# Performance work log

Hardware: AMD Instinct MI355X
Metric: run time of the kernel (lower is better)

## Reference

```python
import jax, jax.numpy as jnp
import numpy as np

B, N, H, D = 2, 2048, 8, 64  # batch, seq, heads, out_channels (per-head, incl. time dim)
E = H * 64                   # embed dim = num_heads * in_channels
C = 1.0                      # manifold curvature c
EPS = 1e-8


def setup_inputs() -> dict:
    key = jax.random.key(0)
    ks = jax.random.split(key, 8)
    d_out = H * (D - 1)
    inp = {
        "query_input": jax.random.normal(ks[0], (B, N, E), dtype=jnp.float32),
        "source_input": jax.random.normal(ks[1], (B, N, E), dtype=jnp.float32),
        "Wq_w": jax.random.normal(ks[2], (d_out, E), dtype=jnp.float32) * 0.02,
        "Wq_b": jnp.zeros((d_out,), dtype=jnp.float32),
        "Wk_w": jax.random.normal(ks[3], (d_out, E), dtype=jnp.float32) * 0.02,
        "Wk_b": jnp.zeros((d_out,), dtype=jnp.float32),
        "Wv_w": jax.random.normal(ks[4], (d_out, E), dtype=jnp.float32) * 0.02,
        "Wv_b": jnp.zeros((d_out,), dtype=jnp.float32),
        "scale": jnp.array([np.sqrt(H * D)], dtype=jnp.float32),
        "bias": jnp.zeros((), dtype=jnp.float32),
    }
    return inp


def _lift(x_space):
    # project space coords onto hyperboloid: prepend time = sqrt(||x||^2 + c)
    t = jnp.sqrt(jnp.sum(x_space * x_space, axis=-1, keepdims=True) + C)
    return jnp.concatenate([t, x_space], axis=-1)  # [..., D]


def _centroid(ave):
    # Lorentzian centroid normalization: sqrt(c) * ave / sqrt(|<ave,ave>_L|)
    inner = jnp.sum(ave * ave, axis=-1, keepdims=True) - 2.0 * ave[..., :1] ** 2
    denom = jnp.sqrt(jnp.maximum(jnp.abs(inner), EPS))
    return jnp.sqrt(C) * ave / denom


def reference(query_input, source_input, Wq_w, Wq_b, Wk_w, Wk_b, Wv_w, Wv_b, scale, bias):
    def heads(x, W, b):
        return (x @ W.T + b).reshape(B, N, H, D - 1)

    q = _lift(heads(query_input, Wq_w, Wq_b))   # [B,N,H,D]
    k = _lift(heads(source_input, Wk_w, Wk_b))  # [B,N,H,D]
    v = _lift(heads(source_input, Wv_w, Wv_b))  # [B,N,H,D]

    # Lorentzian inner product: negate time component of q
    sign = jnp.concatenate([-jnp.ones((1,), q.dtype), jnp.ones((D - 1,), q.dtype)])
    att = 2.0 * C + 2.0 * jnp.einsum('bnhd,bmhd->bhnm', q * sign, k)  # [B,H,N,N]
    att = att / scale[0] + bias
    w = jax.nn.softmax(att, axis=-1)

    ave = jnp.einsum('bhnm,bmhd->bnhd', w, v)   # weighted sum of values
    out = _centroid(ave)                         # per-head hyperbolic centroid [B,N,H,D]
    out = _centroid(jnp.mean(out, axis=2))       # centroid across heads -> [B,N,D]
    return out
```

## Files before the change

kernel.cpp:

```cpp
#include <hip/hip_runtime.h>
#include <math.h>
#include <stdint.h>

#define BB   2
#define NN   2048
#define HH   8
#define DD   64
#define EE   512
#define DM1  63
#define KSP  4

typedef _Float16 half8  __attribute__((ext_vector_type(8)));
typedef __fp16   fp16x2 __attribute__((ext_vector_type(2)));
typedef float    floatx4 __attribute__((ext_vector_type(4)));

__device__ __forceinline__ uint32_t pkh2(float a, float b) {
    union { fp16x2 h; uint32_t u; } uu;
    uu.h = __builtin_amdgcn_cvt_pkrtz(a, b);
    return uu.u;
}
__device__ __forceinline__ half8 as_half8(uint4 u) {
    union { uint4 u; half8 h; } uu; uu.u = u; return uu.h;
}

__global__ __launch_bounds__(256, 3) void qkv_mfma(
    const float* __restrict__ Xq, const float* __restrict__ Xs,
    const float* __restrict__ Wq, const float* __restrict__ Wk,
    const float* __restrict__ Wv,
    const float* __restrict__ Wqb, const float* __restrict__ Wkb,
    const float* __restrict__ Wvb, const float* __restrict__ scale_p,
    _Float16* __restrict__ q16, _Float16* __restrict__ k16,
    _Float16* __restrict__ vT16)
{
    const int mtb = blockIdx.x;
    const int hp  = blockIdx.y;
    const int mat = blockIdx.z;
    const int t    = threadIdx.x;
    const int w    = t >> 6;
    const int lane = t & 63;
    const int l15  = lane & 15;
    const int quad = lane >> 4;

    __shared__ alignas(16) char smem[27648];
    __shared__ float psum[64][4];
    _Float16 (*Xsh)[72]  = (_Float16(*)[72])smem;
    _Float16 (*Wsh)[72]  = (_Float16(*)[72])(smem + 9216);
    _Float16 (*Osh)[136] = (_Float16(*)[136])(smem + 9216);
    _Float16 (*OshT)[72] = (_Float16(*)[72])(smem + 9216);

    const float* X    = (mat == 0) ? Xq : Xs;
    const float* W    = (mat == 0) ? Wq : (mat == 1 ? Wk : Wv);
    const float* bias = (mat == 0) ? Wqb : (mat == 1 ? Wkb : Wvb);
    const int tok0 = mtb * 64;

    floatx4 acc[4][2];
#pragma unroll
    for (int mt = 0; mt < 4; mt++)
#pragma unroll
        for (int nt = 0; nt < 2; nt++) acc[mt][nt] = (floatx4){0.f,0.f,0.f,0.f};

    float4 pxa[2], pxb[2], pwa[4], pwb[4];
#pragma unroll
    for (int ls = 0; ls < 2; ls++) {
        int g = t + 256 * ls, r = g >> 3, c = g & 7;
        const float* p = X + (size_t)(tok0 + r) * EE + c * 8;
        pxa[ls] = *(const float4*)p;
        pxb[ls] = *(const float4*)(p + 4);
    }
#pragma unroll
    for (int ls = 0; ls < 4; ls++) {
        int g = t + 256 * ls, r = g >> 3, c = g & 7;
        int head = r >> 6, j = r & 63;
        pwa[ls] = make_float4(0.f,0.f,0.f,0.f);
        pwb[ls] = make_float4(0.f,0.f,0.f,0.f);
        if (j < DM1) {
            const float* p = W + (size_t)((hp * 2 + head) * DM1 + j) * EE + c * 8;
            pwa[ls] = *(const float4*)p;
            pwb[ls] = *(const float4*)(p + 4);
        }
    }

    for (int it = 0; it < 8; it++) {
        __syncthreads();
#pragma unroll
        for (int ls = 0; ls < 2; ls++) {
            int g = t + 256 * ls, r = g >> 3, c = g & 7;
            uint4 h;
            h.x = pkh2(pxa[ls].x, pxa[ls].y); h.y = pkh2(pxa[ls].z, pxa[ls].w);
            h.z = pkh2(pxb[ls].x, pxb[ls].y); h.w = pkh2(pxb[ls].z, pxb[ls].w);
            *(uint4*)&Xsh[r][c * 8] = h;
        }
#pragma unroll
        for (int ls = 0; ls < 4; ls++) {
            int g = t + 256 * ls, r = g >> 3, c = g & 7;
            uint4 h;
            h.x = pkh2(pwa[ls].x, pwa[ls].y); h.y = pkh2(pwa[ls].z, pwa[ls].w);
            h.z = pkh2(pwb[ls].x, pwb[ls].y); h.w = pkh2(pwb[ls].z, pwb[ls].w);
            *(uint4*)&Wsh[r][c * 8] = h;
        }
        __syncthreads();
        if (it + 1 < 8) {
            int ek = (it + 1) * 64;
#pragma unroll
            for (int ls = 0; ls < 2; ls++) {
                int g = t + 256 * ls, r = g >> 3, c = g & 7;
                const float* p = X + (size_t)(tok0 + r) * EE + ek + c * 8;
                pxa[ls] = *(const float4*)p;
                pxb[ls] = *(const float4*)(p + 4);
            }
#pragma unroll
            for (int ls = 0; ls < 4; ls++) {
                int g = t + 256 * ls, r = g >> 3, c = g & 7;
                int head = r >> 6, j = r & 63;
                if (j < DM1) {
                    const float* p = W + (size_t)((hp * 2 + head) * DM1 + j) * EE + ek + c * 8;
                    pwa[ls] = *(const float4*)p;
                    pwb[ls] = *(const float4*)(p + 4);
                }
            }
        }
#pragma unroll
        for (int kk = 0; kk < 2; kk++) {
            half8 a[4];
#pragma unroll
            for (int mt = 0; mt < 4; mt++)
                a[mt] = *(const half8*)&Xsh[mt * 16 + l15][kk * 32 + quad * 8];
#pragma unroll
            for (int nt = 0; nt < 2; nt++) {
                half8 bfr = *(const half8*)&Wsh[w * 32 + nt * 16 + l15][kk * 32 + quad * 8];
#pragma unroll
                for (int mt = 0; mt < 4; mt++)
                    acc[mt][nt] = __builtin_amdgcn_mfma_f32_16x16x32_f16(
                        a[mt], bfr, acc[mt][nt], 0, 0, 0);
            }
        }
    }
    __syncthreads();

    const float st   = 2.0f / scale_p[0];
    const float fmul = (mat == 0) ? st : 1.0f;

    float vals[4][2][4];
    float sqp[4][4];
#pragma unroll
    for (int mt = 0; mt < 4; mt++)
#pragma unroll
        for (int r = 0; r < 4; r++) sqp[mt][r] = 0.f;

#pragma unroll
    for (int mt = 0; mt < 4; mt++)
#pragma unroll
        for (int nt = 0; nt < 2; nt++) {
            int col = w * 32 + nt * 16 + l15;
            int head = col >> 6, j = col & 63;
            float bb = (j < DM1) ? bias[(hp * 2 + head) * DM1 + j] : 0.f;
#pragma unroll
            for (int r = 0; r < 4; r++) {
                float vv = acc[mt][nt][r] + bb;
                if (j >= DM1) vv = 0.f;
                vals[mt][nt][r] = vv;
                sqp[mt][r] += vv * vv;
            }
        }
#pragma unroll
    for (int mt = 0; mt < 4; mt++)
#pragma unroll
        for (int r = 0; r < 4; r++) {
            float s = sqp[mt][r];
            s += __shfl_xor(s, 1, 64); s += __shfl_xor(s, 2, 64);
            s += __shfl_xor(s, 4, 64); s += __shfl_xor(s, 8, 64);
            if (l15 == 0) psum[mt * 16 + quad * 4 + r][w] = s;
        }

    if (mat < 2) {
#pragma unroll
        for (int mt = 0; mt < 4; mt++)
#pragma unroll
            for (int nt = 0; nt < 2; nt++) {
                int col = w * 32 + nt * 16 + l15;
                int head = col >> 6, j = col & 63;
                if (j < DM1) {
                    int dc = head * 64 + 1 + j;
#pragma unroll
                    for (int r = 0; r < 4; r++)
                        Osh[mt * 16 + quad * 4 + r][dc] = (_Float16)(vals[mt][nt][r] * fmul);
                }
            }
    } else {
#pragma unroll
        for (int mt = 0; mt < 4; mt++)
#pragma unroll
            for (int nt = 0; nt < 2; nt++) {
                int col = w * 32 + nt * 16 + l15;
                uint2 pu;
                pu.x = pkh2(vals[mt][nt][0], vals[mt][nt][1]);
                pu.y = pkh2(vals[mt][nt][2], vals[mt][nt][3]);
                *(uint2*)&OshT[col][mt * 16 + quad * 4] = pu;
            }
    }
    __syncthreads();
    if (t < 64) {
        float tsA = sqrtf(psum[t][0] + psum[t][1] + 1.0f);
        float tsB = sqrtf(psum[t][2] + psum[t][3] + 1.0f);
        if (mat < 2) {
            float tm = (mat == 0) ? -st : 1.0f;
            Osh[t][0]  = (_Float16)(tsA * tm);
            Osh[t][64] = (_Float16)(tsB * tm);
        } else {
            OshT[63][t]  = (_Float16)tsA;
            OshT[127][t] = (_Float16)tsB;
        }
    }
    __syncthreads();

    const int bI = tok0 >> 11, n0 = tok0 & 2047;
    if (mat < 2) {
        _Float16* O = (mat == 0) ? q16 : k16;
#pragma unroll
        for (int ls = 0; ls < 4; ls++) {
            int s = t + 256 * ls, r = s >> 4, c = s & 15, head = c >> 3;
            size_t bh = (size_t)(bI * HH + hp * 2 + head);
            *(uint4*)&O[(bh * NN + n0 + r) * DD + (c & 7) * 8] = *(const uint4*)&Osh[r][c * 8];
        }
    } else {
#pragma unroll
        for (int ls = 0; ls < 4; ls++) {
            int s = t + 256 * ls, df = s >> 3, c = s & 7;
            int head = df >> 6, d = df & 63;
            int rr = head * 64 + ((d + 63) & 63);
            size_t bh = (size_t)(bI * HH + hp * 2 + head);
            uint4 v = *(const uint4*)&OshT[rr][c * 8];
            int cc = c & 3, hf = c >> 2;
            int sA = hf * 32 + ((2 * cc) & 3) * 8 + (cc >> 1) * 4;
            int sB = hf * 32 + ((2 * cc + 1) & 3) * 8 + (cc >> 1) * 4;
            _Float16* vrow = &vT16[(bh * DD + d) * NN + n0];
            *(uint2*)&vrow[sA] = make_uint2(v.x, v.y);
            *(uint2*)&vrow[sB] = make_uint2(v.z, v.w);
        }
    }
}

__global__ __launch_bounds__(256, 2) void lorentz_attn_v11(
    const _Float16* __restrict__ q16, const _Float16* __restrict__ k16,
    const _Float16* __restrict__ vT16,
    _Float16* __restrict__ Odh, float* __restrict__ Ors)
{
    const int qt = blockIdx.x;
    const int bh = blockIdx.y;
    const int ks = blockIdx.z;
    const int t    = threadIdx.x;
    const int w    = t >> 6;
    const int lane = t & 63;
    const int l15  = lane & 15;
    const int quad = lane >> 4;

    __shared__ alignas(16) char smem[36864];

    const _Float16* kb = k16  + (size_t)bh * NN * DD;
    const _Float16* vb = vT16 + (size_t)bh * DD * NN;
    const int base = ks * 8;

    half8 qb[4][2];
#pragma unroll
    for (int mt = 0; mt < 4; mt++) {
        const _Float16* qrow = q16 +
            ((size_t)bh * NN + qt * 256 + w * 64 + mt * 16 + l15) * DD;
        qb[mt][0] = *(const half8*)&qrow[quad * 8];
        qb[mt][1] = *(const half8*)&qrow[32 + quad * 8];
    }

    half8 vones;
#pragma unroll
    for (int i = 0; i < 8; i++) vones[i] = (_Float16)1.0f;

    uint4 pk[2], pv[2];
#pragma unroll
    for (int ls = 0; ls < 2; ls++) {
        int s = t + 256 * ls, r = s >> 3, c = s & 7;
        pk[ls] = *(const uint4*)&kb[((size_t)base * 64 + r) * DD + c * 8];
        pv[ls] = *(const uint4*)&vb[(size_t)r * NN + base * 64 + c * 8];
    }
#pragma unroll
    for (int ls = 0; ls < 2; ls++) {
        int s = t + 256 * ls, r = s >> 3, c = s & 7;
        *(uint4*)(smem +         (size_t)r * 144 + c * 16) = pk[ls];
        *(uint4*)(smem + 18432 + (size_t)r * 144 + c * 16) = pv[ls];
    }
    __syncthreads();

    floatx4 oacc[4][5];
#pragma unroll
    for (int mt = 0; mt < 4; mt++)
#pragma unroll
        for (int nt = 0; nt < 5; nt++) oacc[mt][nt] = (floatx4){0.f,0.f,0.f,0.f};

    for (int i = 0; i < 8; i++) {
        const int kt = base + i;
        const int buf = i & 1;
        _Float16 (*Ks)[72]  = (_Float16(*)[72])(smem + buf * 9216);
        _Float16 (*VTs)[72] = (_Float16(*)[72])(smem + 18432 + buf * 9216);

        if (i + 1 < 8) {
#pragma unroll
            for (int ls = 0; ls < 2; ls++) {
                int s = t + 256 * ls, r = s >> 3, c = s & 7;
                pk[ls] = *(const uint4*)&kb[((size_t)(kt + 1) * 64 + r) * DD + c * 8];
                pv[ls] = *(const uint4*)&vb[(size_t)r * NN + (kt + 1) * 64 + c * 8];
            }
        }

#pragma unroll
        for (int half = 0; half < 2; half++) {
            floatx4 sacc[2][4];
#pragma unroll
            for (int nt2 = 0; nt2 < 2; nt2++) {
#pragma unroll
                for (int mt = 0; mt < 4; mt++) sacc[nt2][mt] = (floatx4){0.f,0.f,0.f,0.f};
                const int nt = half * 2 + nt2;
#pragma unroll
                for (int kk = 0; kk < 2; kk++) {
                    half8 kf = *(const half8*)&Ks[nt * 16 + l15][kk * 32 + quad * 8];
#pragma unroll
                    for (int mt = 0; mt < 4; mt++)
                        sacc[nt2][mt] = __builtin_amdgcn_mfma_f32_16x16x32_f16(
                            kf, qb[mt][kk], sacc[nt2][mt], 0, 0, 0);
                }
            }
            half8 pa[4];
#pragma unroll
            for (int mt = 0; mt < 4; mt++) {
                uint4 u;
                u.x = pkh2(__expf(sacc[0][mt][0]), __expf(sacc[0][mt][1]));
                u.y = pkh2(__expf(sacc[0][mt][2]), __expf(sacc[0][mt][3]));
                u.z = pkh2(__expf(sacc[1][mt][0]), __expf(sacc[1][mt][1]));
                u.w = pkh2(__expf(sacc[1][mt][2]), __expf(sacc[1][mt][3]));
                pa[mt] = as_half8(u);
            }
#pragma unroll
            for (int nt = 0; nt < 4; nt++) {
                half8 vf = *(const half8*)&VTs[nt * 16 + l15][half * 32 + quad * 8];
#pragma unroll
                for (int mt = 0; mt < 4; mt++)
                    oacc[mt][nt] = __builtin_amdgcn_mfma_f32_16x16x32_f16(
                        pa[mt], vf, oacc[mt][nt], 0, 0, 0);
            }
#pragma unroll
            for (int mt = 0; mt < 4; mt++)
                oacc[mt][4] = __builtin_amdgcn_mfma_f32_16x16x32_f16(
                    pa[mt], vones, oacc[mt][4], 0, 0, 0);
        }

        if (i + 1 < 8) {
            char* kd = smem +         (1 - buf) * 9216;
            char* vd = smem + 18432 + (1 - buf) * 9216;
#pragma unroll
            for (int ls = 0; ls < 2; ls++) {
                int s = t + 256 * ls, r = s >> 3, c = s & 7;
                *(uint4*)(kd + (size_t)r * 144 + c * 16) = pk[ls];
                *(uint4*)(vd + (size_t)r * 144 + c * 16) = pv[ls];
            }
        }
        __syncthreads();
    }

    const size_t obase = (((size_t)ks * 16 + bh) * NN + qt * 256 + w * 64);
    float* slab = (float*)(smem + w * 4608);
#pragma unroll
    for (int mt = 0; mt < 4; mt++) {
#pragma unroll
        for (int nt = 0; nt < 4; nt++)
#pragma unroll
            for (int r = 0; r < 4; r++)
                slab[(quad * 4 + r) * 68 + nt * 16 + l15] = oacc[mt][nt][r];
#pragma unroll
        for (int i = 0; i < 4; i++) {
            int s = lane + 64 * i, row = s >> 4, c4 = (s & 15) * 4;
            float4 v = *(const float4*)&slab[row * 68 + c4];
            uint2 pu;
            pu.x = pkh2(v.x, v.y);
            pu.y = pkh2(v.z, v.w);
            *(uint2*)&Odh[(obase + mt * 16 + row) * 64 + c4] = pu;
        }
        if (l15 == 0) {
#pragma unroll
            for (int r = 0; r < 4; r++)
                Ors[obase + mt * 16 + quad * 4 + r] = oacc[mt][4][r];
        }
    }
}

__global__ __launch_bounds__(256) void merge_centroid(
    const _Float16* __restrict__ Odh, const float* __restrict__ Ors,
    float* __restrict__ out)
{
    const int t    = threadIdx.x;
    const int tok  = blockIdx.x * 4 + (t >> 6);
    const int lane = t & 63;
    const int b = tok >> 11;
    const int n = tok & 2047;

    float m = 0.f;
#pragma unroll
    for (int h = 0; h < HH; h++) {
        const size_t bh = (size_t)(b * HH + h);
        float o = 0.f, rs = 0.f;
#pragma unroll
        for (int ksp = 0; ksp < KSP; ksp++) {
            const size_t row = ((size_t)ksp * 16 + bh) * NN + n;
            o  += (float)Odh[row * 64 + lane];
            rs += Ors[row];
        }
        float a  = o / rs;
        float ssq = a * a;
#pragma unroll
        for (int off = 32; off > 0; off >>= 1)
            ssq += __shfl_xor(ssq, off, 64);
        float a0 = __shfl(a, 0, 64);
        float inner = ssq - 2.0f * a0 * a0;
        float f = rsqrtf(fmaxf(fabsf(inner), 1e-8f));
        m += a * f;
    }
    m *= 0.125f;

    float sq = m * m;
#pragma unroll
    for (int off = 32; off > 0; off >>= 1)
        sq += __shfl_xor(sq, off, 64);
    float m0 = __shfl(m, 0, 64);
    float inner = sq - 2.0f * m0 * m0;
    float f = rsqrtf(fmaxf(fabsf(inner), 1e-8f));
    out[(size_t)tok * DD + lane] = m * f;
}

extern "C" void kernel_launch(void* const* d_in, const int* in_sizes, int n_in,
                              void* d_out, int out_size, void* d_ws, size_t ws_size,
                              hipStream_t stream)
{
    const float* Xq  = (const float*)d_in[0];
    const float* Xs  = (const float*)d_in[1];
    const float* Wq  = (const float*)d_in[2];
    const float* Wqb = (const float*)d_in[3];
    const float* Wk  = (const float*)d_in[4];
    const float* Wkb = (const float*)d_in[5];
    const float* Wv  = (const float*)d_in[6];
    const float* Wvb = (const float*)d_in[7];
    const float* sc  = (const float*)d_in[8];
    float* out = (float*)d_out;

    const size_t QSZ = (size_t)BB * HH * NN * DD;
    _Float16* q16  = (_Float16*)d_ws;
    _Float16* k16  = q16 + QSZ;
    _Float16* vT16 = k16 + QSZ;
    _Float16* Odh  = vT16 + QSZ;
    float* Ors = (float*)(Odh + (size_t)KSP * 16 * NN * 64);

    qkv_mfma<<<dim3(64, 4, 3), 256, 0, stream>>>(Xq, Xs, Wq, Wk, Wv,
                                                 Wqb, Wkb, Wvb, sc,
                                                 q16, k16, vT16);
    lorentz_attn_v11<<<dim3(8, 16, KSP), 256, 0, stream>>>(q16, k16, vT16, Odh, Ors);
    merge_centroid<<<(BB * NN) / 4, 256, 0, stream>>>(Odh, Ors, out);
}
```

Baseline: 126.4 us.

## Load QKV weight fragments straight to registers and double-buffer X tiles

In the QKV projection kernel, each wave now loads its own weight B-fragments from global memory directly into registers in MFMA layout and converts them to fp16 there. This drops the shared-memory stage for W. The X tile becomes double-buffered in LDS, which cuts the barriers per K step from two to one and lets the next tile's store overlap the current MFMAs. The cost is redundant global weight reads across waves and blocks, since each wave loads its 32 columns per block, plus more registers held per thread. The attention kernel is only renamed.

Result: slower. 135.0 us (+6.8%).

```diff
diff --git a/kernel.cpp b/kernel.cpp
--- a/kernel.cpp
+++ b/kernel.cpp
@@ -41,12 +41,10 @@
     const int l15  = lane & 15;
     const int quad = lane >> 4;
 
-    __shared__ alignas(16) char smem[27648];
+    __shared__ alignas(16) char smem[18432];
     __shared__ float psum[64][4];
-    _Float16 (*Xsh)[72]  = (_Float16(*)[72])smem;
-    _Float16 (*Wsh)[72]  = (_Float16(*)[72])(smem + 9216);
-    _Float16 (*Osh)[136] = (_Float16(*)[136])(smem + 9216);
-    _Float16 (*OshT)[72] = (_Float16(*)[72])(smem + 9216);
+    _Float16 (*Osh)[136] = (_Float16(*)[136])smem;
+    _Float16 (*OshT)[72] = (_Float16(*)[72])smem;
 
     const float* X    = (mat == 0) ? Xq : Xs;
     const float* W    = (mat == 0) ? Wq : (mat == 1 ? Wk : Wv);
@@ -59,7 +57,18 @@
 #pragma unroll
         for (int nt = 0; nt < 2; nt++) acc[mt][nt] = (floatx4){0.f,0.f,0.f,0.f};
 
-    float4 pxa[2], pxb[2], pwa[4], pwb[4];
+    const float* wrow[2];
+    float wmask[2];
+#pragma unroll
+    for (int nt = 0; nt < 2; nt++) {
+        int col = w * 32 + nt * 16 + l15;
+        int head = col >> 6, j = col & 63;
+        wmask[nt] = (j < DM1) ? 1.f : 0.f;
+        int jj = (j < DM1) ? j : 0;
+        wrow[nt] = W + (size_t)((hp * 2 + head) * DM1 + jj) * EE;
+    }
+
+    float4 pxa[2], pxb[2];
 #pragma unroll
     for (int ls = 0; ls < 2; ls++) {
         int g = t + 256 * ls, r = g >> 3, c = g & 7;
@@ -67,38 +76,44 @@
         pxa[ls] = *(const float4*)p;
         pxb[ls] = *(const float4*)(p + 4);
     }
-#pragma unroll
-    for (int ls = 0; ls < 4; ls++) {
+    float4 wfa[2][2], wfb[2][2];
+#pragma unroll
+    for (int nt = 0; nt < 2; nt++)
+#pragma unroll
+        for (int kk = 0; kk < 2; kk++) {
+            const float* p = wrow[nt] + kk * 32 + quad * 8;
+            wfa[nt][kk] = *(const float4*)p;
+            wfb[nt][kk] = *(const float4*)(p + 4);
+        }
+#pragma unroll
+    for (int ls = 0; ls < 2; ls++) {
         int g = t + 256 * ls, r = g >> 3, c = g & 7;
-        int head = r >> 6, j = r & 63;
-        pwa[ls] = make_float4(0.f,0.f,0.f,0.f);
-        pwb[ls] = make_float4(0.f,0.f,0.f,0.f);
-        if (j < DM1) {
-            const float* p = W + (size_t)((hp * 2 + head) * DM1 + j) * EE + c * 8;
-            pwa[ls] = *(const float4*)p;
-            pwb[ls] = *(const float4*)(p + 4);
-        }
-    }
+        uint4 h;
+        h.x = pkh2(pxa[ls].x, pxa[ls].y); h.y = pkh2(pxa[ls].z, pxa[ls].w);
+        h.z = pkh2(pxb[ls].x, pxb[ls].y); h.w = pkh2(pxb[ls].z, pxb[ls].w);
+        *(uint4*)(smem + (size_t)r * 144 + c * 16) = h;
+    }
+    __syncthreads();
 
     for (int it = 0; it < 8; it++) {
-        __syncthreads();
-#pragma unroll
-        for (int ls = 0; ls < 2; ls++) {
-            int g = t + 256 * ls, r = g >> 3, c = g & 7;
-            uint4 h;
-            h.x = pkh2(pxa[ls].x, pxa[ls].y); h.y = pkh2(pxa[ls].z, pxa[ls].w);
-            h.z = pkh2(pxb[ls].x, pxb[ls].y); h.w = pkh2(pxb[ls].z, pxb[ls].w);
-            *(uint4*)&Xsh[r][c * 8] = h;
-        }
-#pragma unroll
-        for (int ls = 0; ls < 4; ls++) {
-            int g = t + 256 * ls, r = g >> 3, c = g & 7;
-            uint4 h;
-            h.x = pkh2(pwa[ls].x, pwa[ls].y); h.y = pkh2(pwa[ls].z, pwa[ls].w);
-            h.z = pkh2(pwb[ls].x, pwb[ls].y); h.w = pkh2(pwb[ls].z, pwb[ls].w);
-            *(uint4*)&Wsh[r][c * 8] = h;
-        }
-        __syncthreads();
+        const int buf = it & 1;
+        _Float16 (*Xsh)[72] = (_Float16(*)[72])(smem + buf * 9216);
+
+        half8 bfr[2][2];
+#pragma unroll
+        for (int nt = 0; nt < 2; nt++) {
+            float m = wmask[nt];
+#pragma unroll
+            for (int kk = 0; kk < 2; kk++) {
+                uint4 u;
+                u.x = pkh2(wfa[nt][kk].x * m, wfa[nt][kk].y * m);
+                u.y = pkh2(wfa[nt][kk].z * m, wfa[nt][kk].w * m);
+                u.z = pkh2(wfb[nt][kk].x * m, wfb[nt][kk].y * m);
+                u.w = pkh2(wfb[nt][kk].z * m, wfb[nt][kk].w * m);
+                bfr[nt][kk] = as_half8(u);
+            }
+        }
+
         if (it + 1 < 8) {
             int ek = (it + 1) * 64;
 #pragma unroll
@@ -109,16 +124,15 @@
                 pxb[ls] = *(const float4*)(p + 4);
             }
 #pragma unroll
-            for (int ls = 0; ls < 4; ls++) {
-                int g = t + 256 * ls, r = g >> 3, c = g & 7;
-                int head = r >> 6, j = r & 63;
-                if (j < DM1) {
-                    const float* p = W + (size_t)((hp * 2 + head) * DM1 + j) * EE + ek + c * 8;
-                    pwa[ls] = *(const float4*)p;
-                    pwb[ls] = *(const float4*)(p + 4);
+            for (int nt = 0; nt < 2; nt++)
+#pragma unroll
+                for (int kk = 0; kk < 2; kk++) {
+                    const float* p = wrow[nt] + ek + kk * 32 + quad * 8;
+                    wfa[nt][kk] = *(const float4*)p;
+                    wfb[nt][kk] = *(const float4*)(p + 4);
                 }
-            }
-        }
+        }
+
 #pragma unroll
         for (int kk = 0; kk < 2; kk++) {
             half8 a[4];
@@ -126,16 +140,26 @@
             for (int mt = 0; mt < 4; mt++)
                 a[mt] = *(const half8*)&Xsh[mt * 16 + l15][kk * 32 + quad * 8];
 #pragma unroll
-            for (int nt = 0; nt < 2; nt++) {
-                half8 bfr = *(const half8*)&Wsh[w * 32 + nt * 16 + l15][kk * 32 + quad * 8];
+            for (int nt = 0; nt < 2; nt++)
 #pragma unroll
                 for (int mt = 0; mt < 4; mt++)
                     acc[mt][nt] = __builtin_amdgcn_mfma_f32_16x16x32_f16(
-                        a[mt], bfr, acc[mt][nt], 0, 0, 0);
-            }
-        }
-    }
-    __syncthreads();
+                        a[mt], bfr[nt][kk], acc[mt][nt], 0, 0, 0);
+        }
+
+        if (it + 1 < 8) {
+            char* xd = smem + (1 - buf) * 9216;
+#pragma unroll
+            for (int ls = 0; ls < 2; ls++) {
+                int g = t + 256 * ls, r = g >> 3, c = g & 7;
+                uint4 h;
+                h.x = pkh2(pxa[ls].x, pxa[ls].y); h.y = pkh2(pxa[ls].z, pxa[ls].w);
+                h.z = pkh2(pxb[ls].x, pxb[ls].y); h.w = pkh2(pxb[ls].z, pxb[ls].w);
+                *(uint4*)(xd + (size_t)r * 144 + c * 16) = h;
+            }
+        }
+        __syncthreads();
+    }
 
     const float st   = 2.0f / scale_p[0];
     const float fmul = (mat == 0) ? st : 1.0f;
@@ -240,7 +264,7 @@
     }
 }
 
-__global__ __launch_bounds__(256, 2) void lorentz_attn_v11(
+__global__ __launch_bounds__(256, 2) void lorentz_attn_v13(
     const _Float16* __restrict__ q16, const _Float16* __restrict__ k16,
     const _Float16* __restrict__ vT16,
     _Float16* __restrict__ Odh, float* __restrict__ Ors)
@@ -457,6 +481,6 @@
     qkv_mfma<<<dim3(64, 4, 3), 256, 0, stream>>>(Xq, Xs, Wq, Wk, Wv,
                                                  Wqb, Wkb, Wvb, sc,
                                                  q16, k16, vT16);
-    lorentz_attn_v11<<<dim3(8, 16, KSP), 256, 0, stream>>>(q16, k16, vT16, Odh, Ors);
+    lorentz_attn_v13<<<dim3(8, 16, KSP), 256, 0, stream>>>(q16, k16, vT16, Odh, Ors);
     merge_centroid<<<(BB * NN) / 4, 256, 0, stream>>>(Odh, Ors, out);
 }
```
